# Kernel tuning notes

Hardware: AMD Instinct MI355X
Metric: run time of the kernel (lower is better)

The kernel has to match this reference:

```python
import jax, jax.numpy as jnp
import numpy as np

N = 8192
D_IN = 60
NUM_CLASSES = 10


def _xavier(key, out_f, in_f):
    limit = float(np.sqrt(6.0 / (in_f + out_f)))
    return jax.random.uniform(key, (out_f, in_f), jnp.float32, -limit, limit)


def setup_inputs() -> dict:
    key = jax.random.key(0)
    ks = jax.random.split(key, 10)
    return {
        "x": jax.random.normal(ks[0], (N, D_IN), jnp.float32),
        "fc1_w": _xavier(ks[1], 32, 60),
        "fc1_b": jnp.zeros((32,), jnp.float32),
        "fc2_w": _xavier(ks[2], 16, 32),
        "fc2_b": jnp.zeros((16,), jnp.float32),
        "fc3_w": _xavier(ks[3], 8, 60),
        "fc3_b": jnp.zeros((8,), jnp.float32),
        "fc6_w": _xavier(ks[4], NUM_CLASSES, 8),
        "fc6_b": jnp.zeros((NUM_CLASSES,), jnp.float32),
        "temp": jnp.float32(1.0) + 0.1 * jax.random.truncated_normal(ks[5], -2.0, 2.0, (), jnp.float32),
        "theta": jnp.float32(1.0) + 0.1 * jax.random.truncated_normal(ks[6], -2.0, 2.0, (), jnp.float32),
    }


def _pairwise_sq_dist(z):
    # z: [N, d] -> [N, N] squared euclidean distances, clamped at 0
    sq = jnp.sum(z * z, axis=1)  # [N]
    dist = sq[:, None] + sq[None, :] - 2.0 * (z @ z.T)
    return jnp.maximum(dist, 0.0)


def reference(x, fc1_w, fc1_b, fc2_w, fc2_b, fc3_w, fc3_b, fc6_w, fc6_b, temp, theta):
    net = x @ fc1_w.T + fc1_b           # [N, 32]
    net = net @ fc2_w.T + fc2_b         # [N, 16]
    A = -_pairwise_sq_dist(net)         # [N, N]
    A = jax.nn.sigmoid(temp * A + theta)
    # A * (1 - I) + I == set diagonal to 1
    A = jnp.fill_diagonal(A, 1.0, inplace=False)
    A = A / jnp.sum(A, axis=1, keepdims=True)
    h = A @ x                           # [N, 60] dense graph aggregation
    h = h @ fc3_w.T + fc3_b             # [N, 8]
    return jax.nn.softmax(h @ fc6_w.T + fc6_b, axis=1)  # [N, num_classes]
```

## Files before the change

### kernel.cpp

```cpp
#include <hip/hip_runtime.h>
#include <math.h>

#define NROWS 8192
#define DIN   60
#define DZ    16
#define NC    10

#define LOG2E 1.4426950408889634f

#define RB    128
#define CJ    512
#define NRB   (NROWS / RB)
#define NCH   (NROWS / CJ)
#define WAVES 4

typedef short bf16x8 __attribute__((ext_vector_type(8)));
typedef float f32x4  __attribute__((ext_vector_type(4)));

__device__ __forceinline__ unsigned int bfr(float f) {
    return (__float_as_uint(f) + 0x8000u) >> 16;
}

__global__ __launch_bounds__(64) void k1_all(
    const float* __restrict__ x,
    const float* __restrict__ w1, const float* __restrict__ b1,
    const float* __restrict__ w2, const float* __restrict__ b2,
    const float* __restrict__ temp_p, const float* __restrict__ theta_p,
    unsigned short* __restrict__ zb, float* __restrict__ bbf,
    unsigned short* __restrict__ xT)
{
    int i = blockIdx.x * 64 + threadIdx.x;

    float xr[DIN];
    const float4* xp = reinterpret_cast<const float4*>(x + (size_t)i * DIN);
    #pragma unroll
    for (int c = 0; c < 15; ++c) {
        float4 v = xp[c];
        xr[c*4+0] = v.x; xr[c*4+1] = v.y; xr[c*4+2] = v.z; xr[c*4+3] = v.w;
    }

    float n1[32];
    #pragma unroll
    for (int o = 0; o < 32; ++o) {
        float acc = b1[o];
        #pragma unroll
        for (int k = 0; k < DIN; ++k) acc = fmaf(w1[o*DIN+k], xr[k], acc);
        n1[o] = acc;
    }

    float z[DZ];
    float sq = 0.0f;
    #pragma unroll
    for (int u = 0; u < DZ; ++u) {
        float acc = b2[u];
        #pragma unroll
        for (int o = 0; o < 32; ++o) acc = fmaf(w2[u*32+o], n1[o], acc);
        z[u] = acc;
        sq = fmaf(acc, acc, sq);
    }

    float temp  = *temp_p;
    float theta = *theta_p;
    float s = sqrtf(2.0f * temp * LOG2E);

    unsigned int p[8];
    #pragma unroll
    for (int u = 0; u < 8; ++u) {
        unsigned int lo = bfr(z[2*u]   * s);
        unsigned int hi = bfr(z[2*u+1] * s);
        p[u] = lo | (hi << 16);
    }
    uint4* dst = reinterpret_cast<uint4*>(zb + (size_t)i * 32);
    dst[0] = make_uint4(p[0], p[1], p[2], p[3]);
    dst[1] = make_uint4(p[4], p[5], p[6], p[7]);
    dst[2] = make_uint4(0, 0, 0, 0);
    dst[3] = make_uint4(0, 0, 0, 0);

    bbf[i] = LOG2E * fmaf(temp, sq, -0.5f * theta);

    #pragma unroll
    for (int c = 0; c < DIN; ++c)
        xT[(size_t)c * NROWS + i] = (unsigned short)bfr(xr[c]);
    xT[(size_t)60 * NROWS + i] = 0x3F80;
    xT[(size_t)61 * NROWS + i] = 0;
    xT[(size_t)62 * NROWS + i] = 0;
    xT[(size_t)63 * NROWS + i] = 0;
}

__global__ __launch_bounds__(256, 4) void k2_mfma(
    const unsigned short* __restrict__ zb, const float* __restrict__ bbf,
    const unsigned short* __restrict__ xT, const float* __restrict__ theta_p,
    float* __restrict__ hacc)
{
    __shared__ unsigned long long sP[WAVES * 320];

    const int tid  = threadIdx.x;
    const int lane = tid & 63, wave = tid >> 6;
    const int q = lane & 15, g = lane >> 4;
    const int rb = blockIdx.x & (NRB - 1);
    const int ch = blockIdx.x >> 6;
    const int i0 = rb * RB + wave * 32;
    const int j0 = ch * CJ;

    bf16x8 zbi[2];
    float  bi[2];
    #pragma unroll
    for (int t = 0; t < 2; ++t) {
        zbi[t] = *reinterpret_cast<const bf16x8*>(zb + (size_t)(i0 + t*16 + q) * 32 + g*8);
        bi[t]  = bbf[i0 + t*16 + q];
    }
    const float nclamp = -(*theta_p) * LOG2E;
    const f32x4 z4 = {0.0f, 0.0f, 0.0f, 0.0f};

    f32x4 H[2][4];
    #pragma unroll
    for (int t = 0; t < 2; ++t)
        #pragma unroll
        for (int nt = 0; nt < 4; ++nt) H[t][nt] = z4;

    unsigned long long* myP = sP + wave * 320;

    for (int jp = 0; jp < CJ / 32; ++jp) {
        #pragma unroll
        for (int half = 0; half < 2; ++half) {
            const int gj = j0 + jp*32 + half*16;
            bf16x8 za = *reinterpret_cast<const bf16x8*>(zb + (size_t)(gj + q) * 32 + g*8);
            f32x4  bj = *reinterpret_cast<const f32x4*>(bbf + gj + 4*g);
            #pragma unroll
            for (int t = 0; t < 2; ++t) {
                f32x4 S = __builtin_amdgcn_mfma_f32_16x16x32_bf16(za, zbi[t], z4, 0, 0, 0);
                unsigned int ur[4];
                #pragma unroll
                for (int r = 0; r < 4; ++r) {
                    float n = (bi[t] + bj[r]) - S[r];
                    n = fmaxf(n, nclamp);
                    float P = __builtin_amdgcn_rcpf(1.0f + __builtin_amdgcn_exp2f(n));
                    if (i0 + t*16 == gj && q == 4*g + r) P = 0.0f;
                    ur[r] = __float_as_uint(P) + 0x8000u;
                }
                unsigned int pk0 = (ur[0] >> 16) | (ur[1] & 0xFFFF0000u);
                unsigned int pk1 = (ur[2] >> 16) | (ur[3] & 0xFFFF0000u);
                myP[t*160 + q*10 + half*4 + g] =
                    ((unsigned long long)pk1 << 32) | pk0;
            }
        }
        __threadfence_block();

        const int jb = j0 + jp*32;
        bf16x8 pa[2];
        #pragma unroll
        for (int t = 0; t < 2; ++t) {
            union { unsigned long long u[2]; bf16x8 v; } pu;
            pu.u[0] = myP[t*160 + q*10 + g*2];
            pu.u[1] = myP[t*160 + q*10 + g*2 + 1];
            pa[t] = pu.v;
        }
        #pragma unroll
        for (int nt = 0; nt < 4; ++nt) {
            bf16x8 xb = *reinterpret_cast<const bf16x8*>(
                xT + (size_t)(nt*16 + q) * NROWS + jb + g*8);
            H[0][nt] = __builtin_amdgcn_mfma_f32_16x16x32_bf16(pa[0], xb, H[0][nt], 0, 0, 0);
            H[1][nt] = __builtin_amdgcn_mfma_f32_16x16x32_bf16(pa[1], xb, H[1][nt], 0, 0, 0);
        }
    }

    float* regout = hacc + (((size_t)(ch * NRB + rb) * WAVES + wave) * 32) * 64;
    #pragma unroll
    for (int t = 0; t < 2; ++t)
        #pragma unroll
        for (int nt = 0; nt < 4; ++nt)
            #pragma unroll
            for (int r = 0; r < 4; ++r)
                regout[(t*16 + nt*4 + r) * 64 + lane] = H[t][nt][r];
}

#define CHSTRIDE4 (NROWS * 16)

__global__ __launch_bounds__(256) void k3_reduce(
    const float* __restrict__ hacc, float* __restrict__ hfin)
{
    const int T = blockIdx.x * 256 + threadIdx.x;

    const float4* src = reinterpret_cast<const float4*>(hacc) + T;
    float4 s = make_float4(0.0f, 0.0f, 0.0f, 0.0f);
    #pragma unroll 8
    for (int ch = 0; ch < NCH; ++ch) {
        float4 v = src[(size_t)ch * CHSTRIDE4];
        s.x += v.x; s.y += v.y; s.z += v.z; s.w += v.w;
    }

    const int f    = T * 4;
    const int lane = f & 63;
    const int slot = (f >> 6) & 31;
    const int wv   = (f >> 11) & 3;
    const int rb   = f >> 13;
    const int i  = rb * RB + wv * 32 + ((slot >> 4) * 16) + ((lane >> 4) * 4) + (slot & 3);
    const int c0 = ((slot >> 2) & 3) * 16 + (lane & 15);

    *reinterpret_cast<float4*>(hfin + (size_t)i * 64 + c0) = s;
}

__global__ __launch_bounds__(64) void k3_head(
    const float* __restrict__ x,
    const float* __restrict__ w3, const float* __restrict__ b3,
    const float* __restrict__ w6, const float* __restrict__ b6,
    const float* __restrict__ hfin,
    float* __restrict__ out)
{
    int i = blockIdx.x * 64 + threadIdx.x;

    const float* hi = hfin + (size_t)i * 64;
    const float* xi = x + (size_t)i * DIN;

    float rd = __builtin_amdgcn_rcpf(hi[60] + 1.0f);

    float h[DIN];
    #pragma unroll
    for (int k = 0; k < DIN; ++k) h[k] = (hi[k] + xi[k]) * rd;

    float g[8];
    #pragma unroll
    for (int o = 0; o < 8; ++o) {
        float a = b3[o];
        #pragma unroll
        for (int k = 0; k < DIN; ++k) a = fmaf(w3[o*DIN+k], h[k], a);
        g[o] = a;
    }

    float l[NC];
    float m = -3.0e38f;
    #pragma unroll
    for (int c = 0; c < NC; ++c) {
        float a = b6[c];
        #pragma unroll
        for (int o = 0; o < 8; ++o) a = fmaf(w6[c*8+o], g[o], a);
        l[c] = a;
        m = fmaxf(m, a);
    }
    float e[NC];
    float sum = 0.0f;
    #pragma unroll
    for (int c = 0; c < NC; ++c) {
        e[c] = __builtin_amdgcn_exp2f((l[c] - m) * LOG2E);
        sum += e[c];
    }
    float rsum = __builtin_amdgcn_rcpf(sum);
    #pragma unroll
    for (int c = 0; c < NC; ++c) out[(size_t)i * NC + c] = e[c] * rsum;
}

extern "C" void kernel_launch(void* const* d_in, const int* in_sizes, int n_in,
                              void* d_out, int out_size, void* d_ws, size_t ws_size,
                              hipStream_t stream)
{
    const float* x     = (const float*)d_in[0];
    const float* w1    = (const float*)d_in[1];
    const float* b1    = (const float*)d_in[2];
    const float* w2    = (const float*)d_in[3];
    const float* b2    = (const float*)d_in[4];
    const float* w3    = (const float*)d_in[5];
    const float* b3    = (const float*)d_in[6];
    const float* w6    = (const float*)d_in[7];
    const float* b6    = (const float*)d_in[8];
    const float* temp  = (const float*)d_in[9];
    const float* theta = (const float*)d_in[10];
    float* out = (float*)d_out;

    char* p = (char*)d_ws;
    unsigned short* zbuf = (unsigned short*)p;  p += (size_t)NROWS * 32 * 2;
    float*          bbf  = (float*)p;           p += (size_t)NROWS * 4;
    unsigned short* xT   = (unsigned short*)p;  p += (size_t)64 * NROWS * 2;
    float*          hacc = (float*)p;           p += (size_t)NCH * NROWS * 64 * 4;
    float*          hfin = (float*)p;

    k1_all   <<<NROWS / 64, 64, 0, stream>>>(x, w1, b1, w2, b2, temp, theta, zbuf, bbf, xT);
    k2_mfma  <<<NRB * NCH, 256, 0, stream>>>(zbuf, bbf, xT, theta, hacc);
    k3_reduce<<<NROWS * 16 / 256, 256, 0, stream>>>(hacc, hfin);
    k3_head  <<<NROWS / 64, 64, 0, stream>>>(x, w3, b3, w6, b6, hfin, out);
}
```

Measured before the change: 173.5 us.

## Halve split-K chunk, compact z buffer, fuse partial reduction with head

Shrinks the j-chunk per block from 512 to 256 columns, doubling the number of split-K chunks and blocks in the main MFMA kernel. It stores z as 16 bf16 values per row instead of a zero-padded 32 and zero-fills the upper MFMA lanes in registers, which halves z traffic. The separate reduction and head kernels are merged into one kernel that sums the partials into shared memory and runs the head for 16 rows per block. Partial chunks are stored with a padded stride and read in a block-rotated order to spread memory accesses. The trade-off is twice as much partial-accumulator data to write and read, and the fused head uses only 16 of its 256 threads.

```diff
diff --git a/kernel.cpp b/kernel.cpp
--- a/kernel.cpp
+++ b/kernel.cpp
@@ -9,10 +9,12 @@
 #define LOG2E 1.4426950408889634f
 
 #define RB    128
-#define CJ    512
+#define CJ    256
 #define NRB   (NROWS / RB)
 #define NCH   (NROWS / CJ)
 #define WAVES 4
+
+#define CHPAD (NROWS * 64 + 1024)
 
 typedef short bf16x8 __attribute__((ext_vector_type(8)));
 typedef float f32x4  __attribute__((ext_vector_type(4)));
@@ -70,11 +72,9 @@
         unsigned int hi = bfr(z[2*u+1] * s);
         p[u] = lo | (hi << 16);
     }
-    uint4* dst = reinterpret_cast<uint4*>(zb + (size_t)i * 32);
+    uint4* dst = reinterpret_cast<uint4*>(zb + (size_t)i * 16);
     dst[0] = make_uint4(p[0], p[1], p[2], p[3]);
     dst[1] = make_uint4(p[4], p[5], p[6], p[7]);
-    dst[2] = make_uint4(0, 0, 0, 0);
-    dst[3] = make_uint4(0, 0, 0, 0);
 
     bbf[i] = LOG2E * fmaf(temp, sq, -0.5f * theta);
 
@@ -102,11 +102,14 @@
     const int i0 = rb * RB + wave * 32;
     const int j0 = ch * CJ;
 
+    const bf16x8 zero8 = {0,0,0,0,0,0,0,0};
     bf16x8 zbi[2];
     float  bi[2];
     #pragma unroll
     for (int t = 0; t < 2; ++t) {
-        zbi[t] = *reinterpret_cast<const bf16x8*>(zb + (size_t)(i0 + t*16 + q) * 32 + g*8);
+        zbi[t] = (g < 2)
+            ? *reinterpret_cast<const bf16x8*>(zb + (size_t)(i0 + t*16 + q) * 16 + g*8)
+            : zero8;
         bi[t]  = bbf[i0 + t*16 + q];
     }
     const float nclamp = -(*theta_p) * LOG2E;
@@ -124,7 +127,9 @@
         #pragma unroll
         for (int half = 0; half < 2; ++half) {
             const int gj = j0 + jp*32 + half*16;
-            bf16x8 za = *reinterpret_cast<const bf16x8*>(zb + (size_t)(gj + q) * 32 + g*8);
+            bf16x8 za = (g < 2)
+                ? *reinterpret_cast<const bf16x8*>(zb + (size_t)(gj + q) * 16 + g*8)
+                : zero8;
             f32x4  bj = *reinterpret_cast<const f32x4*>(bbf + gj + 4*g);
             #pragma unroll
             for (int t = 0; t < 2; ++t) {
@@ -164,7 +169,8 @@
         }
     }
 
-    float* regout = hacc + (((size_t)(ch * NRB + rb) * WAVES + wave) * 32) * 64;
+    float* regout = hacc + (size_t)ch * CHPAD
+                  + (((size_t)(rb * WAVES + wave)) * 32) * 64;
     #pragma unroll
     for (int t = 0; t < 2; ++t)
         #pragma unroll
@@ -174,79 +180,78 @@
                 regout[(t*16 + nt*4 + r) * 64 + lane] = H[t][nt][r];
 }
 
-#define CHSTRIDE4 (NROWS * 16)
-
-__global__ __launch_bounds__(256) void k3_reduce(
-    const float* __restrict__ hacc, float* __restrict__ hfin)
-{
-    const int T = blockIdx.x * 256 + threadIdx.x;
-
-    const float4* src = reinterpret_cast<const float4*>(hacc) + T;
-    float4 s = make_float4(0.0f, 0.0f, 0.0f, 0.0f);
-    #pragma unroll 8
-    for (int ch = 0; ch < NCH; ++ch) {
-        float4 v = src[(size_t)ch * CHSTRIDE4];
-        s.x += v.x; s.y += v.y; s.z += v.z; s.w += v.w;
-    }
-
-    const int f    = T * 4;
-    const int lane = f & 63;
-    const int slot = (f >> 6) & 31;
-    const int wv   = (f >> 11) & 3;
-    const int rb   = f >> 13;
-    const int i  = rb * RB + wv * 32 + ((slot >> 4) * 16) + ((lane >> 4) * 4) + (slot & 3);
-    const int c0 = ((slot >> 2) & 3) * 16 + (lane & 15);
-
-    *reinterpret_cast<float4*>(hfin + (size_t)i * 64 + c0) = s;
-}
-
-__global__ __launch_bounds__(64) void k3_head(
+__global__ __launch_bounds__(256) void k3_fused(
+    const float* __restrict__ hacc,
     const float* __restrict__ x,
     const float* __restrict__ w3, const float* __restrict__ b3,
     const float* __restrict__ w6, const float* __restrict__ b6,
-    const float* __restrict__ hfin,
     float* __restrict__ out)
 {
-    int i = blockIdx.x * 64 + threadIdx.x;
-
-    const float* hi = hfin + (size_t)i * 64;
-    const float* xi = x + (size_t)i * DIN;
-
-    float rd = __builtin_amdgcn_rcpf(hi[60] + 1.0f);
-
-    float h[DIN];
-    #pragma unroll
-    for (int k = 0; k < DIN; ++k) h[k] = (hi[k] + xi[k]) * rd;
-
-    float g[8];
-    #pragma unroll
-    for (int o = 0; o < 8; ++o) {
-        float a = b3[o];
-        #pragma unroll
-        for (int k = 0; k < DIN; ++k) a = fmaf(w3[o*DIN+k], h[k], a);
-        g[o] = a;
-    }
-
-    float l[NC];
-    float m = -3.0e38f;
-    #pragma unroll
-    for (int c = 0; c < NC; ++c) {
-        float a = b6[c];
-        #pragma unroll
-        for (int o = 0; o < 8; ++o) a = fmaf(w6[c*8+o], g[o], a);
-        l[c] = a;
-        m = fmaxf(m, a);
-    }
-    float e[NC];
-    float sum = 0.0f;
-    #pragma unroll
-    for (int c = 0; c < NC; ++c) {
-        e[c] = __builtin_amdgcn_exp2f((l[c] - m) * LOG2E);
-        sum += e[c];
-    }
-    float rsum = __builtin_amdgcn_rcpf(sum);
-    #pragma unroll
-    for (int c = 0; c < NC; ++c) out[(size_t)i * NC + c] = e[c] * rsum;
+    __shared__ float sh[16][64];
+
+    const int tid = threadIdx.x;
+    const int b   = blockIdx.x;
+
+    {
+        const float4* src = reinterpret_cast<const float4*>(
+            hacc + (size_t)b * 1024) + tid;
+        float4 s = make_float4(0.0f, 0.0f, 0.0f, 0.0f);
+        #pragma unroll 8
+        for (int cc = 0; cc < NCH; ++cc) {
+            int ch = (cc + b) & (NCH - 1);
+            float4 v = src[(size_t)ch * (CHPAD / 4)];
+            s.x += v.x; s.y += v.y; s.z += v.z; s.w += v.w;
+        }
+        const int f    = tid * 4;
+        const int lane = f & 63;
+        const int slt  = (f >> 6) & 15;
+        const int il   = (lane >> 4) * 4 + (slt & 3);
+        const int cl   = ((slt >> 2) & 3) * 16 + (lane & 15);
+        *reinterpret_cast<float4*>(&sh[il][cl]) = s;
+    }
+    __syncthreads();
+
+    if (tid < 16) {
+        const int row = b * 16 + tid;
+        const float* hi = sh[tid];
+        const float* xi = x + (size_t)row * DIN;
+
+        float rd = __builtin_amdgcn_rcpf(hi[60] + 1.0f);
+
+        float h[DIN];
+        #pragma unroll
+        for (int k = 0; k < DIN; ++k) h[k] = (hi[k] + xi[k]) * rd;
+
+        float g[8];
+        #pragma unroll
+        for (int o = 0; o < 8; ++o) {
+            float a = b3[o];
+            #pragma unroll
+            for (int k = 0; k < DIN; ++k) a = fmaf(w3[o*DIN+k], h[k], a);
+            g[o] = a;
+        }
+
+        float l[NC];
+        float m = -3.0e38f;
+        #pragma unroll
+        for (int c = 0; c < NC; ++c) {
+            float a = b6[c];
+            #pragma unroll
+            for (int o = 0; o < 8; ++o) a = fmaf(w6[c*8+o], g[o], a);
+            l[c] = a;
+            m = fmaxf(m, a);
+        }
+        float e[NC];
+        float sum = 0.0f;
+        #pragma unroll
+        for (int c = 0; c < NC; ++c) {
+            e[c] = __builtin_amdgcn_exp2f((l[c] - m) * LOG2E);
+            sum += e[c];
+        }
+        float rsum = __builtin_amdgcn_rcpf(sum);
+        #pragma unroll
+        for (int c = 0; c < NC; ++c) out[(size_t)row * NC + c] = e[c] * rsum;
+    }
 }
 
 extern "C" void kernel_launch(void* const* d_in, const int* in_sizes, int n_in,
@@ -267,14 +272,12 @@
     float* out = (float*)d_out;
 
     char* p = (char*)d_ws;
-    unsigned short* zbuf = (unsigned short*)p;  p += (size_t)NROWS * 32 * 2;
+    unsigned short* zbuf = (unsigned short*)p;  p += (size_t)NROWS * 16 * 2;
     float*          bbf  = (float*)p;           p += (size_t)NROWS * 4;
     unsigned short* xT   = (unsigned short*)p;  p += (size_t)64 * NROWS * 2;
-    float*          hacc = (float*)p;           p += (size_t)NCH * NROWS * 64 * 4;
-    float*          hfin = (float*)p;
-
-    k1_all   <<<NROWS / 64, 64, 0, stream>>>(x, w1, b1, w2, b2, temp, theta, zbuf, bbf, xT);
-    k2_mfma  <<<NRB * NCH, 256, 0, stream>>>(zbuf, bbf, xT, theta, hacc);
-    k3_reduce<<<NROWS * 16 / 256, 256, 0, stream>>>(hacc, hfin);
-    k3_head  <<<NROWS / 64, 64, 0, stream>>>(x, w3, b3, w6, b6, hfin, out);
-}
+    float*          hacc = (float*)p;
+
+    k1_all  <<<NROWS / 64, 64, 0, stream>>>(x, w1, b1, w2, b2, temp, theta, zbuf, bbf, xT);
+    k2_mfma <<<NRB * NCH, 256, 0, stream>>>(zbuf, bbf, xT, theta, hacc);
+    k3_fused<<<NROWS / 16, 256, 0, stream>>>(hacc, x, w3, b3, w6, b6, out);
+}
```

Result: slower. 179.9 us (+3.7%).
